# Performance work log

Hardware: AMD Instinct MI355X
Metric: run time of the kernel (lower is better)

The kernel has to match this reference:

```python
import jax, jax.numpy as jnp
import numpy as np

B, S_RAW, S_SUM, D_IN, H, NH = 32, 1024, 128, 300, 256, 4
DH = (2 * H) // NH  # per-head dim = 128


def _lstm_dir(x, Wih, Whh, b, reverse):
    """Single-direction LSTM (PyTorch gate order i,f,g,o). x: [B,S,D] -> [B,S,H]."""
    xg = jnp.einsum('bsd,gd->bsg', x, Wih) + b          # precompute input gates [B,S,4H]
    xg = jnp.swapaxes(xg, 0, 1)                          # [S,B,4H]
    Hh = Whh.shape[1]
    bsz = x.shape[0]

    def step(carry, g):
        h, c = carry
        gates = g + h @ Whh.T
        i, f, gg, o = jnp.split(gates, 4, axis=-1)
        c = jax.nn.sigmoid(f) * c + jax.nn.sigmoid(i) * jnp.tanh(gg)
        h = jax.nn.sigmoid(o) * jnp.tanh(c)
        return (h, c), h

    init = (jnp.zeros((bsz, Hh), x.dtype), jnp.zeros((bsz, Hh), x.dtype))
    _, hs = jax.lax.scan(step, init, xg, reverse=reverse)  # hs aligned with input time order
    return jnp.swapaxes(hs, 0, 1)


def _bilstm(x, pf, pb):
    return jnp.concatenate([_lstm_dir(x, *pf, False), _lstm_dir(x, *pb, True)], axis=-1)


def setup_inputs() -> dict:
    key = jax.random.key(0)
    ks = jax.random.split(key, 24)
    s_lstm = 1.0 / np.sqrt(H)
    s_proj = 1.0 / np.sqrt(2 * H)
    d = {}
    d['in_raw'] = jax.random.normal(ks[0], (B, S_RAW, D_IN), jnp.float32)
    d['in_sum'] = jax.random.normal(ks[1], (B, S_SUM, D_IN), jnp.float32)
    d['len_raw'] = jax.random.randint(ks[2], (B,), 0, S_RAW)
    d['len_sum'] = jax.random.randint(ks[3], (B,), 0, S_SUM)
    i = 4
    for name in ['raw_f', 'raw_b', 'sum_f', 'sum_b']:
        d[name + '_Wih'] = jax.random.uniform(ks[i], (4 * H, D_IN), jnp.float32, -s_lstm, s_lstm); i += 1
        d[name + '_Whh'] = jax.random.uniform(ks[i], (4 * H, H), jnp.float32, -s_lstm, s_lstm); i += 1
        d[name + '_b'] = jax.random.uniform(ks[i], (4 * H,), jnp.float32, -s_lstm, s_lstm); i += 1
    d['Wq'] = jax.random.uniform(ks[i], (NH, 2 * H, DH), jnp.float32, -s_proj, s_proj); i += 1
    d['Wk'] = jax.random.uniform(ks[i], (NH, 2 * H, DH), jnp.float32, -s_proj, s_proj); i += 1
    d['Wv'] = jax.random.uniform(ks[i], (NH, 2 * H, DH), jnp.float32, -s_proj, s_proj)
    return d


def reference(in_raw, in_sum, len_raw, len_sum,
              raw_f_Wih, raw_f_Whh, raw_f_b, raw_b_Wih, raw_b_Whh, raw_b_b,
              sum_f_Wih, sum_f_Whh, sum_f_b, sum_b_Wih, sum_b_Whh, sum_b_b,
              Wq, Wk, Wv):
    # BiLSTM encoders (dropout is identity in eval mode)
    out_raw = _bilstm(in_raw, (raw_f_Wih, raw_f_Whh, raw_f_b), (raw_b_Wih, raw_b_Whh, raw_b_b))  # [B,Sr,2H]
    out_sum = _bilstm(in_sum, (sum_f_Wih, sum_f_Whh, sum_f_b), (sum_b_Wih, sum_b_Whh, sum_b_b))  # [B,Ss,2H]

    # mean_pooling over the first len_sum[i] timesteps (lengths clamped to >=1)
    lens = jnp.maximum(len_sum, 1)
    mask = (jnp.arange(S_SUM)[None, :] < lens[:, None]).astype(out_sum.dtype)  # [B,Ss]
    sum_vec = jnp.einsum('bsd,bs->bd', out_sum, mask) / lens.astype(out_sum.dtype)[:, None]  # [B,2H]

    # per-head cross-attention against the single pooled summary vector (rank-1 attention)
    q = jnp.einsum('bsd,hde->hbse', out_raw, Wq)   # [NH,B,Sr,DH]
    k = jnp.einsum('bd,hde->hbe', sum_vec, Wk)     # [NH,B,DH]
    v = jnp.einsum('bd,hde->hbe', sum_vec, Wv)     # [NH,B,DH]
    scores = jnp.einsum('hbse,hbe->hbs', q, k)     # [NH,B,Sr] (use_divide_dk=False)
    attn = jax.nn.softmax(scores, axis=-1)
    rst = attn[..., None] * v[:, :, None, :] + q   # outer product + residual, [NH,B,Sr,DH]

    # concat heads along last dim -> [B,Sr,2H]
    rst = jnp.transpose(rst, (1, 2, 0, 3)).reshape(B, S_RAW, NH * DH)
    return rst
```

## Files before the change

kernel.cpp:

```cpp
#include <hip/hip_runtime.h>

typedef _Float16 f16;
typedef _Float16 half2t __attribute__((ext_vector_type(2)));
typedef _Float16 half8 __attribute__((ext_vector_type(8)));
typedef float f32x4 __attribute__((ext_vector_type(4)));

#define KP 320
#define DIN 300
#define SRAW 1024
#define SSUM 128

static constexpr size_t OFF_XG_RAW  = 0;
static constexpr size_t OFF_XG_SUM  = OFF_XG_RAW + (size_t)2*32*1024*1024*2;
static constexpr size_t OFF_OUT_RAW = OFF_XG_SUM + (size_t)2*32*128*1024*2;
static constexpr size_t OFF_OUT_SUM = OFF_OUT_RAW + (size_t)32*1024*512*2;
static constexpr size_t OFF_A_RAW   = OFF_OUT_SUM + (size_t)32*128*512*2;
static constexpr size_t OFF_A_SUM   = OFF_A_RAW + (size_t)32768*KP*2;
static constexpr size_t OFF_BIH_RAW = OFF_A_SUM + (size_t)4096*KP*2;
static constexpr size_t OFF_BIH_SUM = OFF_BIH_RAW + (size_t)2048*KP*2;
static constexpr size_t OFF_WHH     = OFF_BIH_SUM + (size_t)2048*KP*2;
static constexpr size_t OFF_WQ      = OFF_WHH + (size_t)4*32*1024*8*2;
static constexpr size_t OFF_KB      = OFF_WQ + (size_t)512*512*2;
static constexpr size_t OFF_VB      = OFF_KB + (size_t)4*32*128*4;
static constexpr size_t OFF_ATTN    = OFF_VB + (size_t)4*32*128*4;
static constexpr size_t WS_NEED     = OFF_ATTN + (size_t)4*32*1024*4;

__global__ void pack_kernel(
    const float* __restrict__ in_raw, const float* __restrict__ in_sum,
    const float* __restrict__ wih_rf, const float* __restrict__ wih_rb,
    const float* __restrict__ wih_sf, const float* __restrict__ wih_sb,
    const float* __restrict__ whh_rf, const float* __restrict__ whh_rb,
    const float* __restrict__ whh_sf, const float* __restrict__ whh_sb,
    const float* __restrict__ wq,
    f16* __restrict__ a_raw, f16* __restrict__ a_sum,
    f16* __restrict__ bih_raw, f16* __restrict__ bih_sum,
    f16* __restrict__ whh16, f16* __restrict__ wq16)
{
  constexpr size_t N1 = (size_t)32768*KP;
  constexpr size_t N2 = (size_t)4096*KP;
  constexpr size_t N3 = (size_t)2048*KP;
  constexpr size_t N5 = (size_t)4*32*1024*8;
  constexpr size_t N6 = (size_t)512*512;
  const size_t TOT = N1+N2+N3+N3+N5+N6;
  const size_t stride = (size_t)gridDim.x*blockDim.x;
  for (size_t i = (size_t)blockIdx.x*blockDim.x + threadIdx.x; i < TOT; i += stride) {
    size_t j = i;
    if (j < N1) {
      size_t m = j/KP, k = j - m*KP;
      a_raw[j] = (f16)(k < DIN ? in_raw[m*DIN + k] : 0.f);
      continue;
    }
    j -= N1;
    if (j < N2) {
      size_t m = j/KP, k = j - m*KP;
      a_sum[j] = (f16)(k < DIN ? in_sum[m*DIN + k] : 0.f);
      continue;
    }
    j -= N2;
    if (j < N3) {
      size_t n = j/KP, k = j - n*KP;
      float v = 0.f;
      if (k < DIN) v = (n < 1024) ? wih_rf[n*DIN + k] : wih_rb[(n-1024)*DIN + k];
      bih_raw[j] = (f16)v;
      continue;
    }
    j -= N3;
    if (j < N3) {
      size_t n = j/KP, k = j - n*KP;
      float v = 0.f;
      if (k < DIN) v = (n < 1024) ? wih_sf[n*DIN + k] : wih_sb[(n-1024)*DIN + k];
      bih_sum[j] = (f16)v;
      continue;
    }
    j -= N3;
    if (j < N5) {
      int ed = (int)(j >> 18);
      int c  = (int)((j >> 13) & 31);
      int t  = (int)((j >> 3) & 1023);
      int ii = (int)(j & 7);
      int jrow = c >> 2, q = c & 3;
      int rg = t >> 3, ks = t & 7;
      int row = rg*8 + jrow;
      int col = ks*32 + q*8 + ii;
      const float* src = (ed==0)?whh_rf:(ed==1)?whh_rb:(ed==2)?whh_sf:whh_sb;
      whh16[j] = (f16)src[(size_t)row*256 + col];
      continue;
    }
    j -= N5;
    {
      int n = (int)(j >> 9), k = (int)(j & 511);
      int h = n >> 7, dh = n & 127;
      wq16[j] = (f16)wq[((size_t)h*512 + k)*128 + dh];
    }
  }
}

template<int EPI>
__global__ __launch_bounds__(256) void gemm_kernel(
    const f16* __restrict__ A, const f16* __restrict__ Bm,
    float* __restrict__ Cf, f16* __restrict__ Cx,
    const float* __restrict__ bias0, const float* __restrict__ bias1,
    int K, int ldcN, size_t dirStride)
{
  __shared__ __align__(16) f16 As[128*40];
  __shared__ __align__(16) f16 Bs[128*40];
  const int tid = threadIdx.x;
  const int m0 = blockIdx.x*128, n0 = blockIdx.y*128;
  const int w = tid >> 6, lane = tid & 63;
  const int wm = w >> 1, wn = w & 1;
  const int lr = lane & 15, lk = lane >> 4;
  f32x4 acc[4][4] = {};
  const int nsteps = K >> 5;
  for (int kt = 0; kt < nsteps; ++kt) {
    __syncthreads();
    #pragma unroll
    for (int it = 0; it < 2; ++it) {
      int c = tid + it*256;
      int r = c >> 2, kc = c & 3;
      *(uint4*)&As[r*40 + kc*8] = *(const uint4*)&A[(size_t)(m0+r)*K + kt*32 + kc*8];
      *(uint4*)&Bs[r*40 + kc*8] = *(const uint4*)&Bm[(size_t)(n0+r)*K + kt*32 + kc*8];
    }
    __syncthreads();
    half8 af[4], bf[4];
    #pragma unroll
    for (int mt = 0; mt < 4; ++mt) af[mt] = *(const half8*)&As[(wm*64 + mt*16 + lr)*40 + lk*8];
    #pragma unroll
    for (int nt = 0; nt < 4; ++nt) bf[nt] = *(const half8*)&Bs[(wn*64 + nt*16 + lr)*40 + lk*8];
    #pragma unroll
    for (int mt = 0; mt < 4; ++mt)
      #pragma unroll
      for (int nt = 0; nt < 4; ++nt)
        acc[mt][nt] = __builtin_amdgcn_mfma_f32_16x16x32_f16(af[mt], bf[nt], acc[mt][nt], 0, 0, 0);
  }
  const int rb = lk*4;
  #pragma unroll
  for (int mt = 0; mt < 4; ++mt) {
    #pragma unroll
    for (int nt = 0; nt < 4; ++nt) {
      int n = n0 + wn*64 + nt*16 + lr;
      int mloc = m0 + wm*64 + mt*16 + rb;
      if (EPI == 0) {
        #pragma unroll
        for (int r = 0; r < 4; ++r)
          Cf[(size_t)(mloc+r)*ldcN + n] = acc[mt][nt][r];
      } else {
        int dir = n >> 10, cc = n & 1023;
        float bs = (dir ? bias1 : bias0)[cc];
        f16* dst = Cx + (size_t)dir*dirStride;
        #pragma unroll
        for (int r = 0; r < 4; ++r)
          dst[(size_t)(mloc+r)*1024 + cc] = (f16)(acc[mt][nt][r] + bs);
      }
    }
  }
}


__device__ __forceinline__ float dot8(float acc, uint4 wv, uint4 hv) {
#if __has_builtin(__builtin_amdgcn_fdot2)
  union { uint4 u; half2t h[4]; } W, Hh;
  W.u = wv; Hh.u = hv;
  #pragma unroll
  for (int i = 0; i < 4; ++i) acc = __builtin_amdgcn_fdot2(W.h[i], Hh.h[i], acc, false);
#else
  union { uint4 u; f16 h[8]; } W, Hh;
  W.u = wv; Hh.u = hv;
  #pragma unroll
  for (int i = 0; i < 8; ++i) acc += (float)W.h[i]*(float)Hh.h[i];
#endif
  return acc;
}

__device__ __forceinline__ float sigmoid_f(float x) {
  float e = __expf(-x);
  return __builtin_amdgcn_rcpf(1.f + e);
}
__device__ __forceinline__ float tanh_f(float x) {
  float e = __expf(2.f * x);
  return 1.f - 2.f * __builtin_amdgcn_rcpf(e + 1.f);
}

__device__ __forceinline__ void pin4(uint4& v) {
  asm volatile("" : "+v"(v.x), "+v"(v.y), "+v"(v.z), "+v"(v.w));
}

template<int CTRL>
__device__ __forceinline__ float dpp_add(float v) {
  int m = __builtin_amdgcn_update_dpp(0, __builtin_bit_cast(int, v), CTRL, 0xf, 0xf, true);
  return v + __builtin_bit_cast(float, m);
}
__device__ __forceinline__ float reduce8(float v) {
  v = dpp_add<0xB1>(v);
  v = dpp_add<0x4E>(v);
  v = dpp_add<0x141>(v);
  return v;
}

__global__ void __launch_bounds__(1024) __attribute__((amdgpu_waves_per_eu(4, 4)))
lstm_kernel(
    const f16* __restrict__ whh16,
    const f16* __restrict__ xg_raw, const f16* __restrict__ xg_sum,
    f16* __restrict__ out_raw, f16* __restrict__ out_sum)
{
  const int wg = blockIdx.x;
  const int e = wg >> 6, r2 = wg & 63, d = r2 >> 5, b = r2 & 31;
  const int S = e ? SSUM : SRAW;
  const int t = threadIdx.x;
  const int ks = t & 7;
  const uint4* wb = (const uint4*)(whh16 + (size_t)(e*2+d)*(32*1024*8));
  const f16* xg = (e ? xg_sum : xg_raw) + ((size_t)(d*32 + b))*(size_t)S*1024;
  f16* outp = (e ? out_sum : out_raw) + (size_t)b*S*512 + d*256;

  __shared__ __align__(16) uint4 wl[2*4*1024];
  __shared__ float pre[1024];
  __shared__ __align__(16) f16 hl[256];

  #pragma unroll
  for (int c = 0; c < 8; ++c) wl[c*1024 + t] = wb[(24 + c)*1024 + t];
  uint4 wr[24];
  #pragma unroll
  for (int c = 0; c < 24; ++c) wr[c] = wb[c*1024 + t];
  #pragma unroll
  for (int c = 0; c < 24; ++c) pin4(wr[c]);

  if (t < 256) hl[t] = (f16)0.f;
  float cst = 0.f;
  const int hbyte = ks*64;
  const bool isG = ((t >> 8) == 2);
  __syncthreads();

  for (int st = 0; st < S; ++st) {
    const int s = d ? (S - 1 - st) : st;

    float xv = (float)xg[(size_t)s*1024 + t];

    uint4 hv[4];
    #pragma unroll
    for (int q = 0; q < 4; ++q)
      hv[q] = *(const uint4*)((const char*)hl + hbyte + q*16);

    float pa = 0.f;

    #pragma unroll
    for (int j = 0; j < 6; ++j) {
      float rs = 0.f;
      #pragma unroll
      for (int q = 0; q < 4; ++q) rs = dot8(rs, wr[j*4 + q], hv[q]);
      rs = reduce8(rs);
      pa = (ks == j) ? rs : pa;
    }
    #pragma unroll
    for (int jj = 0; jj < 2; ++jj) {
      float rs = 0.f;
      #pragma unroll
      for (int q = 0; q < 4; ++q) rs = dot8(rs, wl[(jj*4 + q)*1024 + t], hv[q]);
      rs = reduce8(rs);
      pa = (ks == 6 + jj) ? rs : pa;
    }

    float v = pa + xv;
    pre[t] = isG ? tanh_f(v) : sigmoid_f(v);
    __syncthreads();

    if (t < 256) {
      float ig = pre[t], fg = pre[256 + t], gg = pre[512 + t], og = pre[768 + t];
      cst = fg*cst + ig*gg;
      float hval = og*tanh_f(cst);
      f16 hf = (f16)hval;
      hl[t] = hf;
      outp[(size_t)s*512 + t] = hf;
    }
    __syncthreads();
  }
}

__global__ __launch_bounds__(256) void pool_kv_kernel(
    const f16* __restrict__ out_sum, const int* __restrict__ len_sum,
    const float* __restrict__ Wk, const float* __restrict__ Wv,
    float* __restrict__ kb, float* __restrict__ vb)
{
  const int b = blockIdx.x, t = threadIdx.x;
  __shared__ float sv[512];
  int len = len_sum[b]; if (len < 1) len = 1;
  float a0 = 0.f, a1 = 0.f;
  for (int s = 0; s < len; ++s) {
    const f16* row = out_sum + ((size_t)b*SSUM + s)*512;
    a0 += (float)row[t];
    a1 += (float)row[t+256];
  }
  float inv = 1.f/(float)len;
  sv[t] = a0*inv; sv[t+256] = a1*inv;
  __syncthreads();
  #pragma unroll
  for (int half = 0; half < 2; ++half) {
    int o = t + half*256;
    int h = o >> 7, dh = o & 127;
    const float* wkp = Wk + (size_t)h*512*128 + dh;
    const float* wvp = Wv + (size_t)h*512*128 + dh;
    float ak = 0.f, av = 0.f;
    for (int e2 = 0; e2 < 512; ++e2) {
      float sve = sv[e2];
      ak += sve*wkp[(size_t)e2*128];
      av += sve*wvp[(size_t)e2*128];
    }
    kb[((size_t)h*32 + b)*128 + dh] = ak;
    vb[((size_t)h*32 + b)*128 + dh] = av;
  }
}

__global__ __launch_bounds__(256) void attn_kernel(
    const float* __restrict__ q, const float* __restrict__ kb, float* __restrict__ attn)
{
  const int hb = blockIdx.x;
  const int h = hb >> 5, b = hb & 31;
  const int t = threadIdx.x;
  __shared__ __align__(16) float kk[128];
  __shared__ float red[4];
  if (t < 128) kk[t] = kb[(size_t)hb*128 + t];
  __syncthreads();
  float vals[4];
  #pragma unroll
  for (int i = 0; i < 4; ++i) {
    int s = t + i*256;
    const float4* qp = (const float4*)(q + ((size_t)b*1024 + s)*512 + h*128);
    const float4* kp = (const float4*)kk;
    float a = 0.f;
    #pragma unroll
    for (int e2 = 0; e2 < 32; ++e2) {
      float4 qq = qp[e2], kx = kp[e2];
      a += qq.x*kx.x + qq.y*kx.y + qq.z*kx.z + qq.w*kx.w;
    }
    vals[i] = a;
  }
  float m = fmaxf(fmaxf(vals[0], vals[1]), fmaxf(vals[2], vals[3]));
  for (int o = 1; o < 64; o <<= 1) m = fmaxf(m, __shfl_xor(m, o));
  if ((t & 63) == 0) red[t >> 6] = m;
  __syncthreads();
  m = fmaxf(fmaxf(red[0], red[1]), fmaxf(red[2], red[3]));
  __syncthreads();
  float ex[4], lsum = 0.f;
  #pragma unroll
  for (int i = 0; i < 4; ++i) { ex[i] = __expf(vals[i] - m); lsum += ex[i]; }
  for (int o = 1; o < 64; o <<= 1) lsum += __shfl_xor(lsum, o);
  if ((t & 63) == 0) red[t >> 6] = lsum;
  __syncthreads();
  float inv = 1.f/(red[0] + red[1] + red[2] + red[3]);
  #pragma unroll
  for (int i = 0; i < 4; ++i) attn[(size_t)hb*1024 + t + i*256] = ex[i]*inv;
}

__global__ __launch_bounds__(256) void final_kernel(
    float* __restrict__ out, const float* __restrict__ attn, const float* __restrict__ vb)
{
  const size_t TOT4 = (size_t)32*1024*512/4;
  const size_t stride = (size_t)gridDim.x*blockDim.x;
  for (size_t i = (size_t)blockIdx.x*blockDim.x + threadIdx.x; i < TOT4; i += stride) {
    int c4 = (int)(i & 127);
    int h = c4 >> 5;
    size_t srow = i >> 7;
    int b = (int)(srow >> 10), s = (int)(srow & 1023);
    float a = attn[((size_t)h*32 + b)*1024 + s];
    float4 vv = ((const float4*)vb)[((size_t)h*32 + b)*32 + (c4 & 31)];
    float4 qq = ((float4*)out)[i];
    qq.x += a*vv.x; qq.y += a*vv.y; qq.z += a*vv.z; qq.w += a*vv.w;
    ((float4*)out)[i] = qq;
  }
}

extern "C" void kernel_launch(void* const* d_in, const int* in_sizes, int n_in,
                              void* d_out, int out_size, void* d_ws, size_t ws_size,
                              hipStream_t stream)
{
  const float* in_raw = (const float*)d_in[0];
  const float* in_sum = (const float*)d_in[1];
  const int*  len_sum = (const int*)d_in[3];
  const float* rf_wih = (const float*)d_in[4];
  const float* rf_whh = (const float*)d_in[5];
  const float* rf_b   = (const float*)d_in[6];
  const float* rb_wih = (const float*)d_in[7];
  const float* rb_whh = (const float*)d_in[8];
  const float* rb_b   = (const float*)d_in[9];
  const float* sf_wih = (const float*)d_in[10];
  const float* sf_whh = (const float*)d_in[11];
  const float* sf_b   = (const float*)d_in[12];
  const float* sb_wih = (const float*)d_in[13];
  const float* sb_whh = (const float*)d_in[14];
  const float* sb_b   = (const float*)d_in[15];
  const float* wq     = (const float*)d_in[16];
  const float* wk     = (const float*)d_in[17];
  const float* wv     = (const float*)d_in[18];

  if (ws_size < WS_NEED) return;

  char* ws = (char*)d_ws;
  f16* xg_raw_p  = (f16*)(ws + OFF_XG_RAW);
  f16* xg_sum_p  = (f16*)(ws + OFF_XG_SUM);
  f16* out_raw_p = (f16*)(ws + OFF_OUT_RAW);
  f16* out_sum_p = (f16*)(ws + OFF_OUT_SUM);
  f16* a_raw_p   = (f16*)(ws + OFF_A_RAW);
  f16* a_sum_p   = (f16*)(ws + OFF_A_SUM);
  f16* bih_raw_p = (f16*)(ws + OFF_BIH_RAW);
  f16* bih_sum_p = (f16*)(ws + OFF_BIH_SUM);
  f16* whh16_p   = (f16*)(ws + OFF_WHH);
  f16* wq16_p    = (f16*)(ws + OFF_WQ);
  float* kb_p    = (float*)(ws + OFF_KB);
  float* vb_p    = (float*)(ws + OFF_VB);
  float* attn_p  = (float*)(ws + OFF_ATTN);
  float* qout    = (float*)d_out;

  pack_kernel<<<4096, 256, 0, stream>>>(
      in_raw, in_sum, rf_wih, rb_wih, sf_wih, sb_wih,
      rf_whh, rb_whh, sf_whh, sb_whh, wq,
      a_raw_p, a_sum_p, bih_raw_p, bih_sum_p, whh16_p, wq16_p);

  gemm_kernel<1><<<dim3(256, 16), 256, 0, stream>>>(
      a_raw_p, bih_raw_p, nullptr, xg_raw_p, rf_b, rb_b, KP, 0, (size_t)32*1024*1024);
  gemm_kernel<1><<<dim3(32, 16), 256, 0, stream>>>(
      a_sum_p, bih_sum_p, nullptr, xg_sum_p, sf_b, sb_b, KP, 0, (size_t)32*128*1024);

  lstm_kernel<<<128, 1024, 0, stream>>>(whh16_p, xg_raw_p, xg_sum_p, out_raw_p, out_sum_p);

  gemm_kernel<0><<<dim3(256, 4), 256, 0, stream>>>(
      out_raw_p, wq16_p, qout, nullptr, nullptr, nullptr, 512, 512, 0);

  pool_kv_kernel<<<32, 256, 0, stream>>>(out_sum_p, len_sum, wk, wv, kb_p, vb_p);
  attn_kernel<<<128, 256, 0, stream>>>(qout, kb_p, attn_p);
  final_kernel<<<4096, 256, 0, stream>>>(qout, attn_p, vb_p);
}
```

Measured before the change: 2.084 ms.

## Split LSTM recurrence across workgroup pairs with global-memory partial-sum exchange

Each (stream, direction, batch) LSTM recurrence now runs on two 1024-thread workgroups, each holding half of the K dimension of W_hh in registers, so no weights spill to LDS. After each step the two workgroups exchange partial gate sums through a global buffer, using release/acquire flags and a spin-wait. The aim is to use 256 CUs instead of 128 and to halve per-step dot-product work and register pressure. In exchange, every timestep now pays a cross-CU round trip through global memory or L2. The design also depends on both workgroups of a pair being co-resident, or the spin-wait will deadlock.

```diff
diff --git a/kernel.cpp b/kernel.cpp
--- a/kernel.cpp
+++ b/kernel.cpp
@@ -9,6 +9,7 @@
 #define DIN 300
 #define SRAW 1024
 #define SSUM 128
+#define SCOPE_AGENT __HIP_MEMORY_SCOPE_AGENT
 
 static constexpr size_t OFF_XG_RAW  = 0;
 static constexpr size_t OFF_XG_SUM  = OFF_XG_RAW + (size_t)2*32*1024*1024*2;
@@ -19,11 +20,13 @@
 static constexpr size_t OFF_BIH_RAW = OFF_A_SUM + (size_t)4096*KP*2;
 static constexpr size_t OFF_BIH_SUM = OFF_BIH_RAW + (size_t)2048*KP*2;
 static constexpr size_t OFF_WHH     = OFF_BIH_SUM + (size_t)2048*KP*2;
-static constexpr size_t OFF_WQ      = OFF_WHH + (size_t)4*32*1024*8*2;
+static constexpr size_t OFF_WQ      = OFF_WHH + (size_t)4*2*1024*8*16*2;
 static constexpr size_t OFF_KB      = OFF_WQ + (size_t)512*512*2;
 static constexpr size_t OFF_VB      = OFF_KB + (size_t)4*32*128*4;
 static constexpr size_t OFF_ATTN    = OFF_VB + (size_t)4*32*128*4;
 static constexpr size_t WS_NEED     = OFF_ATTN + (size_t)4*32*1024*4;
+static constexpr size_t OFF_XCHG    = OFF_BIH_RAW;
+static constexpr size_t OFF_FLAGS   = OFF_BIH_RAW + (size_t)256*2*1024*4;
 
 __global__ void pack_kernel(
     const float* __restrict__ in_raw, const float* __restrict__ in_sum,
@@ -39,7 +42,7 @@
   constexpr size_t N1 = (size_t)32768*KP;
   constexpr size_t N2 = (size_t)4096*KP;
   constexpr size_t N3 = (size_t)2048*KP;
-  constexpr size_t N5 = (size_t)4*32*1024*8;
+  constexpr size_t N5 = (size_t)4*2*1024*8*16;
   constexpr size_t N6 = (size_t)512*512;
   const size_t TOT = N1+N2+N3+N3+N5+N6;
   const size_t stride = (size_t)gridDim.x*blockDim.x;
@@ -75,13 +78,12 @@
     j -= N3;
     if (j < N5) {
       int ed = (int)(j >> 18);
-      int c  = (int)((j >> 13) & 31);
-      int t  = (int)((j >> 3) & 1023);
-      int ii = (int)(j & 7);
-      int jrow = c >> 2, q = c & 3;
-      int rg = t >> 3, ks = t & 7;
-      int row = rg*8 + jrow;
-      int col = ks*32 + q*8 + ii;
+      int kh = (int)((j >> 17) & 1);
+      int t  = (int)((j >> 7) & 1023);
+      int jr = (int)((j >> 4) & 7);
+      int ii = (int)(j & 15);
+      int row = (t >> 3)*8 + jr;
+      int col = kh*128 + (t & 7)*16 + ii;
       const float* src = (ed==0)?whh_rf:(ed==1)?whh_rb:(ed==2)?whh_sf:whh_sb;
       whh16[j] = (f16)src[(size_t)row*256 + col];
       continue;
@@ -93,6 +95,10 @@
       wq16[j] = (f16)wq[((size_t)h*512 + k)*128 + dh];
     }
   }
+}
+
+__global__ void zero_flags_kernel(unsigned* __restrict__ flags) {
+  flags[blockIdx.x*1024 + threadIdx.x] = 0u;
 }
 
 template<int EPI>
@@ -196,79 +202,84 @@
   return v;
 }
 
-__global__ void __launch_bounds__(1024) __attribute__((amdgpu_waves_per_eu(4, 4)))
+__global__ void __launch_bounds__(1024)
 lstm_kernel(
     const f16* __restrict__ whh16,
     const f16* __restrict__ xg_raw, const f16* __restrict__ xg_sum,
-    f16* __restrict__ out_raw, f16* __restrict__ out_sum)
+    f16* __restrict__ out_raw, f16* __restrict__ out_sum,
+    float* __restrict__ xchg, unsigned* __restrict__ flags)
 {
   const int wg = blockIdx.x;
-  const int e = wg >> 6, r2 = wg & 63, d = r2 >> 5, b = r2 & 31;
+  const int p = wg >> 1, kh = wg & 1;
+  const int e = p >> 6, d = (p >> 5) & 1, b = p & 31;
   const int S = e ? SSUM : SRAW;
   const int t = threadIdx.x;
   const int ks = t & 7;
-  const uint4* wb = (const uint4*)(whh16 + (size_t)(e*2+d)*(32*1024*8));
+
+  const uint4* wb = (const uint4*)whh16 + ((size_t)((e*2+d)*2 + kh)*1024 + t)*16;
   const f16* xg = (e ? xg_sum : xg_raw) + ((size_t)(d*32 + b))*(size_t)S*1024;
   f16* outp = (e ? out_sum : out_raw) + (size_t)b*S*512 + d*256;
 
-  __shared__ __align__(16) uint4 wl[2*4*1024];
-  __shared__ float pre[1024];
+  float* xc_mine    = xchg + (size_t)wg*2048;
+  const float* xc_p = xchg + (size_t)(wg ^ 1)*2048;
+  unsigned* flag_mine    = flags + (size_t)wg*16;
+  const unsigned* flag_p = flags + (size_t)(wg ^ 1)*16;
+
+  __shared__ float preL[1024];
   __shared__ __align__(16) f16 hl[256];
 
-  #pragma unroll
-  for (int c = 0; c < 8; ++c) wl[c*1024 + t] = wb[(24 + c)*1024 + t];
-  uint4 wr[24];
-  #pragma unroll
-  for (int c = 0; c < 24; ++c) wr[c] = wb[c*1024 + t];
-  #pragma unroll
-  for (int c = 0; c < 24; ++c) pin4(wr[c]);
+  uint4 wr[16];
+  #pragma unroll
+  for (int c = 0; c < 16; ++c) wr[c] = wb[c];
+  #pragma unroll
+  for (int c = 0; c < 16; ++c) pin4(wr[c]);
 
   if (t < 256) hl[t] = (f16)0.f;
   float cst = 0.f;
-  const int hbyte = ks*64;
+  const int hbyte = kh*256 + ks*32;
   const bool isG = ((t >> 8) == 2);
   __syncthreads();
 
   for (int st = 0; st < S; ++st) {
     const int s = d ? (S - 1 - st) : st;
+    const int par = st & 1;
 
     float xv = (float)xg[(size_t)s*1024 + t];
 
-    uint4 hv[4];
-    #pragma unroll
-    for (int q = 0; q < 4; ++q)
-      hv[q] = *(const uint4*)((const char*)hl + hbyte + q*16);
-
-    float pa = 0.f;
-
-    #pragma unroll
-    for (int j = 0; j < 6; ++j) {
-      float rs = 0.f;
-      #pragma unroll
-      for (int q = 0; q < 4; ++q) rs = dot8(rs, wr[j*4 + q], hv[q]);
+    uint4 hv0 = *(const uint4*)((const char*)hl + hbyte);
+    uint4 hv1 = *(const uint4*)((const char*)hl + hbyte + 16);
+
+    float po = 0.f;
+    #pragma unroll
+    for (int j = 0; j < 8; ++j) {
+      float rs = dot8(0.f, wr[j*2], hv0);
+      rs = dot8(rs, wr[j*2 + 1], hv1);
       rs = reduce8(rs);
-      pa = (ks == j) ? rs : pa;
-    }
-    #pragma unroll
-    for (int jj = 0; jj < 2; ++jj) {
-      float rs = 0.f;
-      #pragma unroll
-      for (int q = 0; q < 4; ++q) rs = dot8(rs, wl[(jj*4 + q)*1024 + t], hv[q]);
-      rs = reduce8(rs);
-      pa = (ks == 6 + jj) ? rs : pa;
-    }
-
-    float v = pa + xv;
-    pre[t] = isG ? tanh_f(v) : sigmoid_f(v);
+      po = (ks == j) ? rs : po;
+    }
+
+    __hip_atomic_store(&xc_mine[par*1024 + t], po, __ATOMIC_RELAXED, SCOPE_AGENT);
+    __syncthreads();
+    if (t == 0) {
+      __threadfence();
+      __hip_atomic_store(flag_mine, (unsigned)(st + 1), __ATOMIC_RELEASE, SCOPE_AGENT);
+      while (__hip_atomic_load(flag_p, __ATOMIC_ACQUIRE, SCOPE_AGENT) < (unsigned)(st + 1))
+        __builtin_amdgcn_s_sleep(2);
+    }
+    __syncthreads();
+
+    float pp = __hip_atomic_load(&xc_p[par*1024 + t], __ATOMIC_RELAXED, SCOPE_AGENT);
+    float v = po + pp + xv;
+    preL[t] = isG ? tanh_f(v) : sigmoid_f(v);
     __syncthreads();
 
     if (t < 256) {
-      float ig = pre[t], fg = pre[256 + t], gg = pre[512 + t], og = pre[768 + t];
+      float ig = preL[t], fg = preL[256 + t], gg = preL[512 + t], og = preL[768 + t];
       cst = fg*cst + ig*gg;
       float hval = og*tanh_f(cst);
       f16 hf = (f16)hval;
       hl[t] = hf;
-      outp[(size_t)s*512 + t] = hf;
+      if (kh == 0) outp[(size_t)s*512 + t] = hf;
     }
     __syncthreads();
   }
@@ -406,6 +417,8 @@
   float* kb_p    = (float*)(ws + OFF_KB);
   float* vb_p    = (float*)(ws + OFF_VB);
   float* attn_p  = (float*)(ws + OFF_ATTN);
+  float* xchg_p  = (float*)(ws + OFF_XCHG);
+  unsigned* flags_p = (unsigned*)(ws + OFF_FLAGS);
   float* qout    = (float*)d_out;
 
   pack_kernel<<<4096, 256, 0, stream>>>(
@@ -418,7 +431,10 @@
   gemm_kernel<1><<<dim3(32, 16), 256, 0, stream>>>(
       a_sum_p, bih_sum_p, nullptr, xg_sum_p, sf_b, sb_b, KP, 0, (size_t)32*128*1024);
 
-  lstm_kernel<<<128, 1024, 0, stream>>>(whh16_p, xg_raw_p, xg_sum_p, out_raw_p, out_sum_p);
+  zero_flags_kernel<<<4, 1024, 0, stream>>>(flags_p);
+
+  lstm_kernel<<<256, 1024, 0, stream>>>(whh16_p, xg_raw_p, xg_sum_p,
+                                        out_raw_p, out_sum_p, xchg_p, flags_p);
 
   gemm_kernel<0><<<dim3(256, 4), 256, 0, stream>>>(
       out_raw_p, wq16_p, qout, nullptr, nullptr, nullptr, 512, 512, 0);
```

After: 7.295 ms. 3.5x slower.

## Shrink LSTM recurrence workgroup to 256 threads with 4 gate rows per thread

Applied to the files above, without the earlier changes.

The recurrent LSTM kernel now runs 256 threads per workgroup instead of 1024. Each group of 8 threads covers 32 weight rows instead of 8, with 29 rows of W_hh held in registers and 3 in LDS, and the repacked weights follow that layout. The hidden-state buffer is padded so the per-k-slice reads avoid bank conflicts, and input gates for the next timestep are prefetched into registers. The aim is cheaper per-step barriers across fewer waves and less LDS weight traffic. In exchange each thread does four times the dot-product work and carries about 464 VGPRs of weights, which risks spilling and a longer serial step.

```diff
diff --git a/kernel.cpp b/kernel.cpp
--- a/kernel.cpp
+++ b/kernel.cpp
@@ -19,7 +19,7 @@
 static constexpr size_t OFF_BIH_RAW = OFF_A_SUM + (size_t)4096*KP*2;
 static constexpr size_t OFF_BIH_SUM = OFF_BIH_RAW + (size_t)2048*KP*2;
 static constexpr size_t OFF_WHH     = OFF_BIH_SUM + (size_t)2048*KP*2;
-static constexpr size_t OFF_WQ      = OFF_WHH + (size_t)4*32*1024*8*2;
+static constexpr size_t OFF_WQ      = OFF_WHH + (size_t)4*128*256*8*2;
 static constexpr size_t OFF_KB      = OFF_WQ + (size_t)512*512*2;
 static constexpr size_t OFF_VB      = OFF_KB + (size_t)4*32*128*4;
 static constexpr size_t OFF_ATTN    = OFF_VB + (size_t)4*32*128*4;
@@ -39,7 +39,7 @@
   constexpr size_t N1 = (size_t)32768*KP;
   constexpr size_t N2 = (size_t)4096*KP;
   constexpr size_t N3 = (size_t)2048*KP;
-  constexpr size_t N5 = (size_t)4*32*1024*8;
+  constexpr size_t N5 = (size_t)4*128*256*8;
   constexpr size_t N6 = (size_t)512*512;
   const size_t TOT = N1+N2+N3+N3+N5+N6;
   const size_t stride = (size_t)gridDim.x*blockDim.x;
@@ -75,12 +75,12 @@
     j -= N3;
     if (j < N5) {
       int ed = (int)(j >> 18);
-      int c  = (int)((j >> 13) & 31);
-      int t  = (int)((j >> 3) & 1023);
+      int c  = (int)((j >> 11) & 127);
+      int t  = (int)((j >> 3) & 255);
       int ii = (int)(j & 7);
       int jrow = c >> 2, q = c & 3;
       int rg = t >> 3, ks = t & 7;
-      int row = rg*8 + jrow;
+      int row = rg*32 + jrow;
       int col = ks*32 + q*8 + ii;
       const float* src = (ed==0)?whh_rf:(ed==1)?whh_rb:(ed==2)?whh_sf:whh_sb;
       whh16[j] = (f16)src[(size_t)row*256 + col];
@@ -155,6 +155,8 @@
   }
 }
 
+#define RROWS 29
+#define LROWS 3
 
 __device__ __forceinline__ float dot8(float acc, uint4 wv, uint4 hv) {
 #if __has_builtin(__builtin_amdgcn_fdot2)
@@ -178,10 +180,6 @@
 __device__ __forceinline__ float tanh_f(float x) {
   float e = __expf(2.f * x);
   return 1.f - 2.f * __builtin_amdgcn_rcpf(e + 1.f);
-}
-
-__device__ __forceinline__ void pin4(uint4& v) {
-  asm volatile("" : "+v"(v.x), "+v"(v.y), "+v"(v.z), "+v"(v.w));
 }
 
 template<int CTRL>
@@ -196,78 +194,92 @@
   return v;
 }
 
-__global__ void __launch_bounds__(1024) __attribute__((amdgpu_waves_per_eu(4, 4)))
+__global__ void __launch_bounds__(256)
 lstm_kernel(
     const f16* __restrict__ whh16,
     const f16* __restrict__ xg_raw, const f16* __restrict__ xg_sum,
     f16* __restrict__ out_raw, f16* __restrict__ out_sum)
 {
   const int wg = blockIdx.x;
-  const int e = wg >> 6, r2 = wg & 63, d = r2 >> 5, b = r2 & 31;
+  const int e = wg >> 6, d = (wg >> 5) & 1, b = wg & 31;
   const int S = e ? SSUM : SRAW;
   const int t = threadIdx.x;
-  const int ks = t & 7;
-  const uint4* wb = (const uint4*)(whh16 + (size_t)(e*2+d)*(32*1024*8));
+  const int rg = t >> 3, ks = t & 7;
+  const uint4* wb = (const uint4*)whh16 + (size_t)(e*2+d)*(128*256);
   const f16* xg = (e ? xg_sum : xg_raw) + ((size_t)(d*32 + b))*(size_t)S*1024;
   f16* outp = (e ? out_sum : out_raw) + (size_t)b*S*512 + d*256;
 
-  __shared__ __align__(16) uint4 wl[2*4*1024];
-  __shared__ float pre[1024];
-  __shared__ __align__(16) f16 hl[256];
-
-  #pragma unroll
-  for (int c = 0; c < 8; ++c) wl[c*1024 + t] = wb[(24 + c)*1024 + t];
-  uint4 wr[24];
-  #pragma unroll
-  for (int c = 0; c < 24; ++c) wr[c] = wb[c*1024 + t];
-  #pragma unroll
-  for (int c = 0; c < 24; ++c) pin4(wr[c]);
-
-  if (t < 256) hl[t] = (f16)0.f;
+  __shared__ __align__(16) uint4 wl[LROWS*4*256];
+  __shared__ float preL[1024];
+  __shared__ __align__(16) char hl8[8*72];
+
+  #pragma unroll
+  for (int c = 0; c < LROWS*4; ++c) wl[c*256 + t] = wb[(RROWS*4 + c)*256 + t];
+  uint4 wr[RROWS*4];
+  #pragma unroll
+  for (int c = 0; c < RROWS*4; ++c) wr[c] = wb[c*256 + t];
+
+  for (int i = t; i < 144; i += 256) ((unsigned*)hl8)[i] = 0u;
   float cst = 0.f;
-  const int hbyte = ks*64;
-  const bool isG = ((t >> 8) == 2);
+  const int hbyte = ks*72;
+  const bool isG = ((t >> 6) == 2);
+  const int row0 = rg*32 + ks;
+
+  const int s0 = d ? (S - 1) : 0;
+  f16 xc[4];
+  #pragma unroll
+  for (int m = 0; m < 4; ++m) xc[m] = xg[(size_t)s0*1024 + row0 + 8*m];
   __syncthreads();
 
   for (int st = 0; st < S; ++st) {
     const int s = d ? (S - 1 - st) : st;
 
-    float xv = (float)xg[(size_t)s*1024 + t];
+    f16 xn[4] = {(f16)0.f, (f16)0.f, (f16)0.f, (f16)0.f};
+    if (st + 1 < S) {
+      const int sn = d ? (S - 2 - st) : (st + 1);
+      #pragma unroll
+      for (int m = 0; m < 4; ++m) xn[m] = xg[(size_t)sn*1024 + row0 + 8*m];
+    }
 
     uint4 hv[4];
     #pragma unroll
     for (int q = 0; q < 4; ++q)
-      hv[q] = *(const uint4*)((const char*)hl + hbyte + q*16);
-
-    float pa = 0.f;
-
-    #pragma unroll
-    for (int j = 0; j < 6; ++j) {
+      hv[q] = *(const uint4*)(hl8 + hbyte + q*16);
+
+    float p[4] = {0.f, 0.f, 0.f, 0.f};
+
+    #pragma unroll
+    for (int j = 0; j < RROWS; ++j) {
       float rs = 0.f;
       #pragma unroll
       for (int q = 0; q < 4; ++q) rs = dot8(rs, wr[j*4 + q], hv[q]);
       rs = reduce8(rs);
-      pa = (ks == j) ? rs : pa;
-    }
-    #pragma unroll
-    for (int jj = 0; jj < 2; ++jj) {
+      if (ks == (j & 7)) p[j >> 3] = rs;
+    }
+    #pragma unroll
+    for (int j = RROWS; j < 32; ++j) {
       float rs = 0.f;
       #pragma unroll
-      for (int q = 0; q < 4; ++q) rs = dot8(rs, wl[(jj*4 + q)*1024 + t], hv[q]);
+      for (int q = 0; q < 4; ++q) rs = dot8(rs, wl[((j - RROWS)*4 + q)*256 + t], hv[q]);
       rs = reduce8(rs);
-      pa = (ks == 6 + jj) ? rs : pa;
-    }
-
-    float v = pa + xv;
-    pre[t] = isG ? tanh_f(v) : sigmoid_f(v);
+      if (ks == (j & 7)) p[j >> 3] = rs;
+    }
+
+    #pragma unroll
+    for (int m = 0; m < 4; ++m) {
+      float v = p[m] + (float)xc[m];
+      float a = isG ? tanh_f(v) : sigmoid_f(v);
+      preL[row0 + 8*m] = a;
+      xc[m] = xn[m];
+    }
     __syncthreads();
 
-    if (t < 256) {
-      float ig = pre[t], fg = pre[256 + t], gg = pre[512 + t], og = pre[768 + t];
+    {
+      float ig = preL[t], fg = preL[256 + t], gg = preL[512 + t], og = preL[768 + t];
       cst = fg*cst + ig*gg;
       float hval = og*tanh_f(cst);
       f16 hf = (f16)hval;
-      hl[t] = hf;
+      *(f16*)(hl8 + (t >> 5)*72 + (t & 31)*2) = hf;
       outp[(size_t)s*512 + t] = hf;
     }
     __syncthreads();
@@ -418,7 +430,7 @@
   gemm_kernel<1><<<dim3(32, 16), 256, 0, stream>>>(
       a_sum_p, bih_sum_p, nullptr, xg_sum_p, sf_b, sb_b, KP, 0, (size_t)32*128*1024);
 
-  lstm_kernel<<<128, 1024, 0, stream>>>(whh16_p, xg_raw_p, xg_sum_p, out_raw_p, out_sum_p);
+  lstm_kernel<<<128, 256, 0, stream>>>(whh16_p, xg_raw_p, xg_sum_p, out_raw_p, out_sum_p);
 
   gemm_kernel<0><<<dim3(256, 4), 256, 0, stream>>>(
       out_raw_p, wq16_p, qout, nullptr, nullptr, nullptr, 512, 512, 0);
```

After: 3.095 ms. 48.5% more time.

## Restructure LSTM recurrence to broadcast h via readlane with SGPR dot2

Applied to the files above, without the earlier changes.

Rewrites the per-step recurrent matvec in the LSTM kernel. Each of 512 threads now owns four gate rows over half of the hidden dimension. The hidden state is broadcast to the wavefront through readlane into scalar registers and consumed by v_dot2 with an SGPR operand, which replaces the DPP cross-lane reductions and the per-lane h loads. The Whh packing layout is changed to match, and the two K-halves are combined through shared memory, which adds one extra barrier per step. The aim is to shorten the serial per-timestep latency, at the cost of 48 pinned uint4 register weights per thread, higher register pressure, and an extra sync.

```diff
diff --git a/kernel.cpp b/kernel.cpp
--- a/kernel.cpp
+++ b/kernel.cpp
@@ -19,7 +19,7 @@
 static constexpr size_t OFF_BIH_RAW = OFF_A_SUM + (size_t)4096*KP*2;
 static constexpr size_t OFF_BIH_SUM = OFF_BIH_RAW + (size_t)2048*KP*2;
 static constexpr size_t OFF_WHH     = OFF_BIH_SUM + (size_t)2048*KP*2;
-static constexpr size_t OFF_WQ      = OFF_WHH + (size_t)4*32*1024*8*2;
+static constexpr size_t OFF_WQ      = OFF_WHH + (size_t)4*8*4*16*64*8*2;
 static constexpr size_t OFF_KB      = OFF_WQ + (size_t)512*512*2;
 static constexpr size_t OFF_VB      = OFF_KB + (size_t)4*32*128*4;
 static constexpr size_t OFF_ATTN    = OFF_VB + (size_t)4*32*128*4;
@@ -39,7 +39,7 @@
   constexpr size_t N1 = (size_t)32768*KP;
   constexpr size_t N2 = (size_t)4096*KP;
   constexpr size_t N3 = (size_t)2048*KP;
-  constexpr size_t N5 = (size_t)4*32*1024*8;
+  constexpr size_t N5 = (size_t)4*8*4*16*64*8;
   constexpr size_t N6 = (size_t)512*512;
   const size_t TOT = N1+N2+N3+N3+N5+N6;
   const size_t stride = (size_t)gridDim.x*blockDim.x;
@@ -75,13 +75,15 @@
     j -= N3;
     if (j < N5) {
       int ed = (int)(j >> 18);
-      int c  = (int)((j >> 13) & 31);
-      int t  = (int)((j >> 3) & 1023);
+      int q  = (int)((j >> 3) & 32767);
       int ii = (int)(j & 7);
-      int jrow = c >> 2, q = c & 3;
-      int rg = t >> 3, ks = t & 7;
-      int row = rg*8 + jrow;
-      int col = ks*32 + q*8 + ii;
+      int l  = q & 63;
+      int c  = (q >> 6) & 15;
+      int m  = (q >> 10) & 3;
+      int w  = (q >> 12) & 7;
+      int rb = w >> 1, kh = w & 1;
+      int row = rb*256 + l + 64*m;
+      int col = kh*128 + c*8 + ii;
       const float* src = (ed==0)?whh_rf:(ed==1)?whh_rb:(ed==2)?whh_sf:whh_sb;
       whh16[j] = (f16)src[(size_t)row*256 + col];
       continue;
@@ -156,18 +158,8 @@
 }
 
 
-__device__ __forceinline__ float dot8(float acc, uint4 wv, uint4 hv) {
-#if __has_builtin(__builtin_amdgcn_fdot2)
-  union { uint4 u; half2t h[4]; } W, Hh;
-  W.u = wv; Hh.u = hv;
-  #pragma unroll
-  for (int i = 0; i < 4; ++i) acc = __builtin_amdgcn_fdot2(W.h[i], Hh.h[i], acc, false);
-#else
-  union { uint4 u; f16 h[8]; } W, Hh;
-  W.u = wv; Hh.u = hv;
-  #pragma unroll
-  for (int i = 0; i < 8; ++i) acc += (float)W.h[i]*(float)Hh.h[i];
-#endif
+__device__ __forceinline__ float sdot2(float acc, unsigned w2, int h2) {
+  asm("v_dot2_f32_f16 %0, %1, %2, %0" : "+v"(acc) : "v"(w2), "s"(h2));
   return acc;
 }
 
@@ -184,86 +176,95 @@
   asm volatile("" : "+v"(v.x), "+v"(v.y), "+v"(v.z), "+v"(v.w));
 }
 
-template<int CTRL>
-__device__ __forceinline__ float dpp_add(float v) {
-  int m = __builtin_amdgcn_update_dpp(0, __builtin_bit_cast(int, v), CTRL, 0xf, 0xf, true);
-  return v + __builtin_bit_cast(float, m);
-}
-__device__ __forceinline__ float reduce8(float v) {
-  v = dpp_add<0xB1>(v);
-  v = dpp_add<0x4E>(v);
-  v = dpp_add<0x141>(v);
-  return v;
-}
-
-__global__ void __launch_bounds__(1024) __attribute__((amdgpu_waves_per_eu(4, 4)))
+__global__ void __launch_bounds__(512, 2)
 lstm_kernel(
     const f16* __restrict__ whh16,
     const f16* __restrict__ xg_raw, const f16* __restrict__ xg_sum,
     f16* __restrict__ out_raw, f16* __restrict__ out_sum)
 {
   const int wg = blockIdx.x;
-  const int e = wg >> 6, r2 = wg & 63, d = r2 >> 5, b = r2 & 31;
+  const int e = wg >> 6, d = (wg >> 5) & 1, b = wg & 31;
   const int S = e ? SSUM : SRAW;
   const int t = threadIdx.x;
-  const int ks = t & 7;
-  const uint4* wb = (const uint4*)(whh16 + (size_t)(e*2+d)*(32*1024*8));
+  const int l = t & 63, w = t >> 6;
+  const int kh = w & 1, rb = w >> 1;
+  const uint4* wb = (const uint4*)whh16 + (size_t)(e*2+d)*32768 + (size_t)w*4096 + l;
   const f16* xg = (e ? xg_sum : xg_raw) + ((size_t)(d*32 + b))*(size_t)S*1024;
   f16* outp = (e ? out_sum : out_raw) + (size_t)b*S*512 + d*256;
 
-  __shared__ __align__(16) uint4 wl[2*4*1024];
-  __shared__ float pre[1024];
-  __shared__ __align__(16) f16 hl[256];
-
-  #pragma unroll
-  for (int c = 0; c < 8; ++c) wl[c*1024 + t] = wb[(24 + c)*1024 + t];
-  uint4 wr[24];
-  #pragma unroll
-  for (int c = 0; c < 24; ++c) wr[c] = wb[c*1024 + t];
-  #pragma unroll
-  for (int c = 0; c < 24; ++c) pin4(wr[c]);
+  __shared__ __align__(16) uint4 wl[16*512];
+  __shared__ float pp[1024];
+  __shared__ float actL[1024];
+  __shared__ __align__(8) f16 hl[256];
+
+  #pragma unroll
+  for (int c = 0; c < 16; ++c) wl[c*512 + t] = wb[(size_t)(3*16 + c)*64];
+  uint4 wr[48];
+  #pragma unroll
+  for (int k = 0; k < 48; ++k) wr[k] = wb[(size_t)k*64];
+  #pragma unroll
+  for (int k = 0; k < 48; ++k) pin4(wr[k]);
 
   if (t < 256) hl[t] = (f16)0.f;
   float cst = 0.f;
-  const int hbyte = ks*64;
-  const bool isG = ((t >> 8) == 2);
+  const int row0 = rb*256 + l;
+  const bool isG = (rb == 2);
   __syncthreads();
 
   for (int st = 0; st < S; ++st) {
     const int s = d ? (S - 1 - st) : st;
 
-    float xv = (float)xg[(size_t)s*1024 + t];
-
-    uint4 hv[4];
-    #pragma unroll
-    for (int q = 0; q < 4; ++q)
-      hv[q] = *(const uint4*)((const char*)hl + hbyte + q*16);
-
-    float pa = 0.f;
-
-    #pragma unroll
-    for (int j = 0; j < 6; ++j) {
-      float rs = 0.f;
-      #pragma unroll
-      for (int q = 0; q < 4; ++q) rs = dot8(rs, wr[j*4 + q], hv[q]);
-      rs = reduce8(rs);
-      pa = (ks == j) ? rs : pa;
-    }
-    #pragma unroll
-    for (int jj = 0; jj < 2; ++jj) {
-      float rs = 0.f;
-      #pragma unroll
-      for (int q = 0; q < 4; ++q) rs = dot8(rs, wl[(jj*4 + q)*1024 + t], hv[q]);
-      rs = reduce8(rs);
-      pa = (ks == 6 + jj) ? rs : pa;
-    }
-
-    float v = pa + xv;
-    pre[t] = isG ? tanh_f(v) : sigmoid_f(v);
+    float xv0 = 0.f, xv1 = 0.f, xv2 = 0.f, xv3 = 0.f;
+    if (kh == 0) {
+      xv0 = (float)xg[(size_t)s*1024 + row0];
+      xv1 = (float)xg[(size_t)s*1024 + row0 + 64];
+      xv2 = (float)xg[(size_t)s*1024 + row0 + 128];
+      xv3 = (float)xg[(size_t)s*1024 + row0 + 192];
+    }
+
+    int hdw = ((const int*)hl)[kh*64 + l];
+
+    float acc0 = 0.f, acc1 = 0.f, acc2 = 0.f, acc3 = 0.f;
+    #pragma unroll
+    for (int c = 0; c < 16; ++c) {
+      uint4 wv3 = wl[c*512 + t];
+      int h0 = __builtin_amdgcn_readlane(hdw, c*4 + 0);
+      int h1 = __builtin_amdgcn_readlane(hdw, c*4 + 1);
+      int h2 = __builtin_amdgcn_readlane(hdw, c*4 + 2);
+      int h3 = __builtin_amdgcn_readlane(hdw, c*4 + 3);
+      uint4 w0 = wr[c], w1 = wr[16 + c], w2 = wr[32 + c];
+      acc0 = sdot2(acc0, w0.x, h0); acc0 = sdot2(acc0, w0.y, h1);
+      acc0 = sdot2(acc0, w0.z, h2); acc0 = sdot2(acc0, w0.w, h3);
+      acc1 = sdot2(acc1, w1.x, h0); acc1 = sdot2(acc1, w1.y, h1);
+      acc1 = sdot2(acc1, w1.z, h2); acc1 = sdot2(acc1, w1.w, h3);
+      acc2 = sdot2(acc2, w2.x, h0); acc2 = sdot2(acc2, w2.y, h1);
+      acc2 = sdot2(acc2, w2.z, h2); acc2 = sdot2(acc2, w2.w, h3);
+      acc3 = sdot2(acc3, wv3.x, h0); acc3 = sdot2(acc3, wv3.y, h1);
+      acc3 = sdot2(acc3, wv3.z, h2); acc3 = sdot2(acc3, wv3.w, h3);
+    }
+
+    if (kh == 1) {
+      pp[row0]       = acc0;
+      pp[row0 + 64]  = acc1;
+      pp[row0 + 128] = acc2;
+      pp[row0 + 192] = acc3;
+    }
     __syncthreads();
 
+    if (kh == 0) {
+      float t0 = acc0 + pp[row0]       + xv0;
+      float t1 = acc1 + pp[row0 + 64]  + xv1;
+      float t2 = acc2 + pp[row0 + 128] + xv2;
+      float t3 = acc3 + pp[row0 + 192] + xv3;
+      actL[row0]       = isG ? tanh_f(t0) : sigmoid_f(t0);
+      actL[row0 + 64]  = isG ? tanh_f(t1) : sigmoid_f(t1);
+      actL[row0 + 128] = isG ? tanh_f(t2) : sigmoid_f(t2);
+      actL[row0 + 192] = isG ? tanh_f(t3) : sigmoid_f(t3);
+    }
+    __syncthreads();
+
     if (t < 256) {
-      float ig = pre[t], fg = pre[256 + t], gg = pre[512 + t], og = pre[768 + t];
+      float ig = actL[t], fg = actL[256 + t], gg = actL[512 + t], og = actL[768 + t];
       cst = fg*cst + ig*gg;
       float hval = og*tanh_f(cst);
       f16 hf = (f16)hval;
@@ -418,7 +419,7 @@
   gemm_kernel<1><<<dim3(32, 16), 256, 0, stream>>>(
       a_sum_p, bih_sum_p, nullptr, xg_sum_p, sf_b, sb_b, KP, 0, (size_t)32*128*1024);
 
-  lstm_kernel<<<128, 1024, 0, stream>>>(whh16_p, xg_raw_p, xg_sum_p, out_raw_p, out_sum_p);
+  lstm_kernel<<<128, 512, 0, stream>>>(whh16_p, xg_raw_p, xg_sum_p, out_raw_p, out_sum_p);
 
   gemm_kernel<0><<<dim3(256, 4), 256, 0, stream>>>(
       out_raw_p, wq16_p, qout, nullptr, nullptr, nullptr, 512, 512, 0);
```

After: 2.449 ms. 1.18x slower.
